# Kernel tuning notes

Measured on AMD Instinct MI355X. Metric: run time of the kernel, lower is better.

Reference implementation:

```python
import jax, jax.numpy as jnp
import numpy as np

F1, F2, F3 = 128, 64, 32
K = 16          # tensor_neurons
BINS = 16
FEAT = K + BINS # feature_count with histogram
BN1, BN2, BN3 = 16, 8, 4
NLAB = 128


def gcn(x, W, b, src, dst, n):
    # PyG GCNConv: h = x W; symmetric norm with self-loops; aggregate at dst.
    h = x @ W
    deg = jax.ops.segment_sum(jnp.ones(src.shape[0], h.dtype), dst, num_segments=n) + 1.0
    dinv = deg ** -0.5
    norm = (dinv[src] * dinv[dst])[:, None]
    agg = jax.ops.segment_sum(h[src] * norm, dst, num_segments=n)
    return agg + h * (dinv ** 2)[:, None] + b  # second term = self-loop


def conv_pass(feat, ei, w1, b1, w2, b2, w3, b3):
    n = feat.shape[0]
    src, dst = ei[0], ei[1]
    h = jax.nn.relu(gcn(feat, w1, b1, src, dst, n))
    h = jax.nn.relu(gcn(h, w2, b2, src, dst, n))
    return gcn(h, w3, b3, src, dst, n)  # [n, F3]


def att_pool(x, W):
    ctx = jnp.tanh(jnp.mean(x @ W, axis=0))      # [F3]
    sig = jax.nn.sigmoid(x @ ctx)                # [n]
    return x.T @ sig                             # [F3]


def histc_norm(a, b):
    # torch.histc with bins over [min, max] of the (detached) scores.
    s = jax.lax.stop_gradient(a @ b.T).reshape(-1)  # [N1*N2]
    lo, hi = s.min(), s.max()
    idx = jnp.clip(jnp.floor((s - lo) / jnp.maximum(hi - lo, 1e-12) * BINS).astype(jnp.int32), 0, BINS - 1)
    h = jax.ops.segment_sum(jnp.ones_like(s), idx, num_segments=BINS)
    return h / h.sum()


def setup_inputs() -> dict:
    key = jax.random.key(0)
    ks = jax.random.split(key, 24)
    N, E = 20000, 640000
    d = {
        'features_1': jax.random.normal(ks[0], (N, NLAB), jnp.float32),
        'features_2': jax.random.normal(ks[1], (N, NLAB), jnp.float32),
        'edge_index_1': jax.random.randint(ks[2], (2, E), 0, N),
        'edge_index_2': jax.random.randint(ks[3], (2, E), 0, N),
        'avg_v': jax.random.uniform(ks[4], (1,), jnp.float32) * 10.0 + 5.0,
    }
    def w(k, shape, fan_in):
        return jax.random.normal(k, shape, jnp.float32) * (1.0 / np.sqrt(fan_in))
    d['w1'] = w(ks[5], (NLAB, F1), NLAB); d['b1'] = jnp.zeros((F1,), jnp.float32)
    d['w2'] = w(ks[6], (F1, F2), F1);     d['b2'] = jnp.zeros((F2,), jnp.float32)
    d['w3'] = w(ks[7], (F2, F3), F2);     d['b3'] = jnp.zeros((F3,), jnp.float32)
    d['attn_w'] = w(ks[8], (F3, F3), F3)
    d['ntn_w'] = w(ks[9], (F3, F3, K), F3)
    d['ntn_v'] = w(ks[10], (K, 2 * F3), 2 * F3)
    d['ntn_b'] = jnp.zeros((K,), jnp.float32)
    d['fc1_w'] = w(ks[11], (FEAT, BN1), FEAT); d['fc1_b'] = jnp.zeros((BN1,), jnp.float32)
    d['fc2_w'] = w(ks[12], (BN1, BN2), BN1);   d['fc2_b'] = jnp.zeros((BN2,), jnp.float32)
    d['fc3_w'] = w(ks[13], (BN2, BN3), BN2);   d['fc3_b'] = jnp.zeros((BN3,), jnp.float32)
    d['score_w'] = w(ks[14], (BN3, 1), BN3);   d['score_b'] = jnp.zeros((1,), jnp.float32)
    return d


def reference(features_1, features_2, avg_v,
              w1, b1, w2, b2, w3, b3,
              attn_w, ntn_w, ntn_v, ntn_b,
              fc1_w, fc1_b, fc2_w, fc2_b, fc3_w, fc3_b,
              score_w, score_b,
              edge_index_1, edge_index_2):
    a1 = conv_pass(features_1, edge_index_1, w1, b1, w2, b2, w3, b3)  # [N1, F3]
    a2 = conv_pass(features_2, edge_index_2, w1, b1, w2, b2, w3, b3)  # [N2, F3]
    p1 = att_pool(a1, attn_w)  # [F3]
    p2 = att_pool(a2, attn_w)  # [F3]
    ntn = jax.nn.relu(jnp.einsum('i,ijk,j->k', p1, ntn_w, p2)
                      + ntn_v @ jnp.concatenate([p1, p2]) + ntn_b)  # [K]
    hist = histc_norm(a1, a2)  # [BINS]
    s = jnp.concatenate([ntn, hist])[None, :]  # [1, FEAT]
    s = jax.nn.relu(s @ fc1_w + fc1_b)
    s = jax.nn.relu(s @ fc2_w + fc2_b)
    s = jax.nn.relu(s @ fc3_w + fc3_b)
    score = jax.nn.sigmoid((s @ score_w + score_b).reshape(-1))  # [1]
    pre_ged = -jnp.log(score) * avg_v  # target_mode == 'exp'
    return score, pre_ged
```

## Files before the change

kernel.cpp:

```cpp
#include <hip/hip_runtime.h>


typedef short s16x8 __attribute__((ext_vector_type(8)));
typedef float f32x4 __attribute__((ext_vector_type(4)));


__global__ __launch_bounds__(256) void count_kern(const int* __restrict__ ei1,
                                                  const int* __restrict__ ei2,
                                                  int* counts, int N, int E)
{
    int g = blockIdx.y;
    const int* dst = (g ? ei2 : ei1) + E;
    int* cnt = counts + (size_t)g * N;
    for (int e = blockIdx.x * 256 + threadIdx.x; e < E; e += gridDim.x * 256)
        atomicAdd(&cnt[dst[e]], 1);
}

__global__ __launch_bounds__(256) void dinv_kern(const int* __restrict__ counts,
                                                 float* dinv, int N)
{
    int g = blockIdx.y;
    int i = blockIdx.x * 256 + threadIdx.x;
    if (i < N) dinv[(size_t)g * N + i] = 1.0f / sqrtf((float)counts[(size_t)g * N + i] + 1.0f);
}

__global__ __launch_bounds__(1024) void scan_kern(const int* __restrict__ counts,
                                                  int* row_ptr, int* cursor, int N)
{
    int g = blockIdx.x;
    const int* cnt = counts + (size_t)g * N;
    int* rp  = row_ptr + (size_t)g * (N + 1);
    int* cur = cursor  + (size_t)g * (N + 1);
    __shared__ int lds[1024];
    int t = threadIdx.x;
    int CH = (N + 1023) >> 10;
    int base = t * CH;
    int sum = 0;
    for (int i = 0; i < CH; i++) {
        int idx = base + i;
        if (idx < N) sum += cnt[idx];
    }
    lds[t] = sum;
    __syncthreads();
    for (int s = 1; s < 1024; s <<= 1) {
        int add = (t >= s) ? lds[t - s] : 0;
        __syncthreads();
        lds[t] += add;
        __syncthreads();
    }
    int run = lds[t] - sum;
    if (t == 0) rp[0] = 0;
    for (int i = 0; i < CH; i++) {
        int idx = base + i;
        if (idx < N) {
            int v = cnt[idx];
            cur[idx] = run;
            run += v;
            rp[idx + 1] = run;
        }
    }
}

__global__ __launch_bounds__(256) void scatter_kern(const int* __restrict__ ei1,
                                                    const int* __restrict__ ei2,
                                                    int* cursor, int* col, int N, int E)
{
    int g = blockIdx.y;
    const int* ei = g ? ei2 : ei1;
    const int* src = ei;
    const int* dst = ei + E;
    int* cur = cursor + (size_t)g * (N + 1);
    int* cl  = col    + (size_t)g * E;
    int e = blockIdx.x * 256 + threadIdx.x;
    if (e < E) {
        int pos = atomicAdd(&cur[dst[e]], 1);
        cl[pos] = src[e];
    }
}


template <int K, int NCOL>
__global__ __launch_bounds__(256) void gemm_kern(const float* __restrict__ xa,
                                                 const float* __restrict__ xb,
                                                 const float* __restrict__ W,
                                                 const float* __restrict__ dinva,
                                                 const float* __restrict__ dinvb,
                                                 float* ya, float* yb, int nodes)
{
    int g = blockIdx.y;
    const float* x = g ? xb : xa;
    const float* dinv = g ? dinvb : dinva;
    float* y = g ? yb : ya;
    constexpr int MB  = 32;
    constexpr int NG  = 256 / NCOL;
    constexpr int RPT = MB / NG;
    __shared__ float xs[MB][K];
    int row0 = blockIdx.x * MB;
    int t = threadIdx.x;
    constexpr int TOT = MB * K / 4;
    for (int i = t; i < TOT; i += 256) {
        int lin = i * 4;
        int r = lin / K, k = lin % K;
        float4 v = make_float4(0.f, 0.f, 0.f, 0.f);
        if (row0 + r < nodes) v = *(const float4*)&x[(size_t)(row0 + r) * K + k];
        *(float4*)&xs[r][k] = v;
    }
    __syncthreads();
    int c  = t % NCOL;
    int rg = t / NCOL;
    float acc[RPT];
#pragma unroll
    for (int i = 0; i < RPT; i++) acc[i] = 0.f;
    for (int k = 0; k < K; k++) {
        float w = W[k * NCOL + c];
#pragma unroll
        for (int i = 0; i < RPT; i++) acc[i] += xs[rg * RPT + i][k] * w;
    }
#pragma unroll
    for (int i = 0; i < RPT; i++) {
        int r = row0 + rg * RPT + i;
        if (r < nodes) y[(size_t)r * NCOL + c] = acc[i] * dinv[r];
    }
}


template <int F, bool RELU>
__global__ __launch_bounds__(256) void agg_kern(const float* __restrict__ ha,
                                                const float* __restrict__ hb,
                                                const int* __restrict__ colA,
                                                const int* __restrict__ colB,
                                                const int* __restrict__ rpA,
                                                const int* __restrict__ rpB,
                                                const float* __restrict__ dinvA,
                                                const float* __restrict__ dinvB,
                                                const float* __restrict__ bias,
                                                float* ya, float* yb, int nodes)
{
    int g = blockIdx.y;
    const float2* hp  = (const float2*)(g ? hb : ha);
    const int*   col  = g ? colB : colA;
    const int*   rp   = g ? rpB : rpA;
    const float* dinv = g ? dinvB : dinvA;
    float2* y = (float2*)(g ? yb : ya);
    constexpr int TPN = F / 2;
    constexpr int NPB = 256 / TPN;
    int t = threadIdx.x;
    int ni = blockIdx.x * NPB + t / TPN;
    int f2 = t % TPN;
    if (ni >= nodes) return;
    int e0 = rp[ni], e1 = rp[ni + 1];
    float ax = 0.f, ay = 0.f;
    for (int e = e0; e < e1; e++) {
        float2 v = hp[(size_t)col[e] * TPN + f2];
        ax += v.x; ay += v.y;
    }
    float2 self = hp[(size_t)ni * TPN + f2];
    float di = dinv[ni];
    float ox = di * (ax + self.x) + bias[2 * f2];
    float oy = di * (ay + self.y) + bias[2 * f2 + 1];
    if (RELU) { ox = fmaxf(ox, 0.f); oy = fmaxf(oy, 0.f); }
    y[(size_t)ni * TPN + f2] = make_float2(ox, oy);
}


__global__ __launch_bounds__(256) void colsum_kern(const float* __restrict__ a1,
                                                   const float* __restrict__ a2,
                                                   float* colsum, int nodes)
{
    int g = blockIdx.y;
    const float* a = g ? a2 : a1;
    float* cs = colsum + g * 32;
    int t = threadIdx.x;
    int c = t & 31, rr = t >> 5;
    float acc = 0.f;
    for (int r = blockIdx.x * 8 + rr; r < nodes; r += gridDim.x * 8)
        acc += a[(size_t)r * 32 + c];
    __shared__ float lds[256];
    lds[t] = acc;
    __syncthreads();
    if (t < 32) {
        float s = 0.f;
#pragma unroll
        for (int j = 0; j < 8; j++) s += lds[j * 32 + t];
        atomicAdd(&cs[t], s);
    }
}

__global__ void ctx_kern(const float* __restrict__ colsum, const float* __restrict__ W,
                         float* ctx, float invN)
{
    int g = blockIdx.x;
    const float* cs = colsum + g * 32;
    int c = threadIdx.x;
    float s = 0.f;
    for (int j = 0; j < 32; j++) s += cs[j] * invN * W[j * 32 + c];
    ctx[g * 32 + c] = tanhf(s);
}

__global__ __launch_bounds__(256) void pool_kern(const float* __restrict__ a1,
                                                 const float* __restrict__ a2,
                                                 const float* __restrict__ ctx,
                                                 float* pooled, int nodes)
{
    int g = blockIdx.y;
    const float* a  = g ? a2 : a1;
    const float* cx = ctx + g * 32;
    float* pl = pooled + g * 32;
    int t = threadIdx.x;
    int c = t & 31, rr = t >> 5;
    float cxc = cx[c];
    float acc = 0.f;
    for (int r = blockIdx.x * 8 + rr; r < nodes; r += gridDim.x * 8) {
        float v = a[(size_t)r * 32 + c];
        float d = v * cxc;
#pragma unroll
        for (int m = 16; m >= 1; m >>= 1) d += __shfl_xor(d, m, 32);
        acc += v * (1.f / (1.f + expf(-d)));
    }
    __shared__ float lds[256];
    lds[t] = acc;
    __syncthreads();
    if (t < 32) {
        float s = 0.f;
#pragma unroll
        for (int j = 0; j < 8; j++) s += lds[j * 32 + t];
        atomicAdd(&pl[t], s);
    }
}


__global__ __launch_bounds__(512) void ntn_kern(const float* __restrict__ pooled,
                                                const float* __restrict__ ntn_w,
                                                const float* __restrict__ ntn_v,
                                                const float* __restrict__ ntn_b,
                                                float* ntn)
{
    const float* p1 = pooled;
    const float* p2 = pooled + 32;
    __shared__ float lds[512];
    int t = threadIdx.x;
    int i = t >> 4, k = t & 15;
    float s = 0.f;
    for (int j = 0; j < 32; j++) s += ntn_w[(i * 32 + j) * 16 + k] * p2[j];
    lds[t] = s * p1[i];
    __syncthreads();
    if (t < 16) {
        float v = 0.f;
        for (int ii = 0; ii < 32; ii++) v += lds[ii * 16 + t];
        for (int j = 0; j < 32; j++) v += ntn_v[t * 64 + j] * p1[j];
        for (int j = 0; j < 32; j++) v += ntn_v[t * 64 + 32 + j] * p2[j];
        v += ntn_b[t];
        ntn[t] = fmaxf(v, 0.f);
    }
}


__device__ __forceinline__ unsigned encf(float f)
{
    unsigned b = __float_as_uint(f);
    return b ^ (unsigned)(((int)b >> 31) | 0x80000000);
}
__device__ __forceinline__ float decf(unsigned u)
{
    unsigned b = (u & 0x80000000u) ? (u ^ 0x80000000u) : ~u;
    return __uint_as_float(b);
}

__device__ __forceinline__ unsigned short f2bf(float f)
{
    unsigned u = __float_as_uint(f);
    return (unsigned short)((u + 0x7FFFu + ((u >> 16) & 1u)) >> 16);
}

__global__ __launch_bounds__(256) void split_kern(const float* __restrict__ a,
                                                  unsigned short* __restrict__ hi,
                                                  unsigned short* __restrict__ lo,
                                                  int total4)
{
    int i = blockIdx.x * 256 + threadIdx.x;
    if (i >= total4) return;
    float4 v = ((const float4*)a)[i];
    ushort4 h, l;
    h.x = f2bf(v.x); l.x = f2bf(v.x - __uint_as_float((unsigned)h.x << 16));
    h.y = f2bf(v.y); l.y = f2bf(v.y - __uint_as_float((unsigned)h.y << 16));
    h.z = f2bf(v.z); l.z = f2bf(v.z - __uint_as_float((unsigned)h.z << 16));
    h.w = f2bf(v.w); l.w = f2bf(v.w - __uint_as_float((unsigned)h.w << 16));
    ((ushort4*)hi)[i] = h;
    ((ushort4*)lo)[i] = l;
}

__device__ __forceinline__ s16x8 ldfrag(const unsigned short* __restrict__ base,
                                        int node0, int lane)
{
    const unsigned short* p = base + (size_t)(node0 + (lane & 15)) * 32 + 8 * (lane >> 4);
    return *(const s16x8*)p;
}

template <int PASS>
__global__ __launch_bounds__(256) void hist_pass(const unsigned short* __restrict__ h1,
                                                 const unsigned short* __restrict__ l1,
                                                 const unsigned short* __restrict__ h2,
                                                 const unsigned short* __restrict__ l2,
                                                 unsigned* encMinArr, unsigned* encMaxArr,
                                                 unsigned* histSub)
{
    int t = threadIdx.x, w = t >> 6, lane = t & 63;
    int row0 = blockIdx.x * 160 + (w >> 1) * 80;
    int col0 = blockIdx.y * 160 + (w & 1) * 80;
    __shared__ unsigned wh[(PASS == 1) ? 4 : 1][16][64];
    __shared__ float bc[2];
    __shared__ unsigned ru[4], rv[4];
    __shared__ float rf[4], rg[4];

    float scale = 0.f, nls = 0.f;
    if (PASS == 1) {
        for (int i = t; i < 4096; i += 256) ((unsigned*)wh)[i] = 0u;
        unsigned mnu = encMinArr[t];
        unsigned mxu = encMaxArr[t];
#pragma unroll
        for (int m = 32; m >= 1; m >>= 1) {
            unsigned a = (unsigned)__shfl_xor((int)mnu, m);
            unsigned b = (unsigned)__shfl_xor((int)mxu, m);
            mnu = a < mnu ? a : mnu;
            mxu = b > mxu ? b : mxu;
        }
        if (lane == 0) { ru[w] = mnu; rv[w] = mxu; }
        __syncthreads();
        if (t == 0) {
            mnu = ru[0]; mxu = rv[0];
#pragma unroll
            for (int j = 1; j < 4; j++) {
                mnu = ru[j] < mnu ? ru[j] : mnu;
                mxu = rv[j] > mxu ? rv[j] : mxu;
            }
            float lof = decf(mnu), hif = decf(mxu);
            bc[0] = lof;
            bc[1] = 16.f / fmaxf(hif - lof, 1e-12f);
        }
        __syncthreads();
        float lo = bc[0];
        scale = bc[1];
        nls = -lo * scale;
    }

    s16x8 ah[5], al[5];
#pragma unroll
    for (int r = 0; r < 5; r++) {
        ah[r] = ldfrag(h1, row0 + r * 16, lane);
        al[r] = ldfrag(l1, row0 + r * 16, lane);
    }
    float mn = 3.4e38f, mx = -3.4e38f;
#pragma unroll
    for (int c = 0; c < 5; c++) {
        s16x8 bh = ldfrag(h2, col0 + c * 16, lane);
        s16x8 bl = ldfrag(l2, col0 + c * 16, lane);
        f32x4 acc[5];
#pragma unroll
        for (int r = 0; r < 5; r++) {
            f32x4 z = {0.f, 0.f, 0.f, 0.f};
            z = __builtin_amdgcn_mfma_f32_16x16x32_bf16(ah[r], bh, z, 0, 0, 0);
            z = __builtin_amdgcn_mfma_f32_16x16x32_bf16(al[r], bh, z, 0, 0, 0);
            z = __builtin_amdgcn_mfma_f32_16x16x32_bf16(ah[r], bl, z, 0, 0, 0);
            acc[r] = z;
        }
#pragma unroll
        for (int r = 0; r < 5; r++)
#pragma unroll
            for (int j = 0; j < 4; j++) {
                float s = acc[r][j];
                if (PASS == 0) {
                    mn = fminf(mn, s);
                    mx = fmaxf(mx, s);
                } else {
                    int bi = (int)fminf(fmaxf(fmaf(s, scale, nls), 0.f), 15.f);
                    atomicAdd(&wh[w][bi][lane], 1u);
                }
            }
    }

    int slot = (int)((blockIdx.x * gridDim.y + blockIdx.y) & 255u);
    if (PASS == 0) {
#pragma unroll
        for (int m = 32; m >= 1; m >>= 1) {
            mn = fminf(mn, __shfl_xor(mn, m));
            mx = fmaxf(mx, __shfl_xor(mx, m));
        }
        if (lane == 0) { rf[w] = mn; rg[w] = mx; }
        __syncthreads();
        if (t == 0) {
            mn = fminf(fminf(rf[0], rf[1]), fminf(rf[2], rf[3]));
            mx = fmaxf(fmaxf(rg[0], rg[1]), fmaxf(rg[2], rg[3]));
            atomicMin(&encMinArr[slot], encf(mn));
            atomicMax(&encMaxArr[slot], encf(mx));
        }
    } else {
        __syncthreads();
        for (int s = 32; s > 0; s >>= 1) {
            for (int idx = t; idx < 4 * 16 * s; idx += 256) {
                int ww  = idx / (16 * s);
                int rem = idx - ww * 16 * s;
                int b   = rem / s;
                int l2i = rem - b * s;
                wh[ww][b][l2i] += wh[ww][b][l2i + s];
            }
            __syncthreads();
        }
        if (t < 16) {
            unsigned tot = wh[0][t][0] + wh[1][t][0] + wh[2][t][0] + wh[3][t][0];
            if (tot) atomicAdd(&histSub[slot * 16 + t], tot);
        }
    }
}


__global__ __launch_bounds__(256) void final_kern(const float* __restrict__ ntn,
                           const unsigned* __restrict__ histSub,
                           const float* __restrict__ fc1w, const float* __restrict__ fc1b,
                           const float* __restrict__ fc2w, const float* __restrict__ fc2b,
                           const float* __restrict__ fc3w, const float* __restrict__ fc3b,
                           const float* __restrict__ scw, const float* __restrict__ scb,
                           const float* __restrict__ avg_v, float* out)
{
    __shared__ unsigned part[256];
    __shared__ float s_fc1w[512];
    __shared__ float s_fc2w[128];
    __shared__ float s_fc3w[32];
    __shared__ float s_fc1b[16], s_fc2b[8], s_fc3b[4], s_scw[4];
    __shared__ float s_feat[32];
    __shared__ float s_h1[16], s_h2[8], s_h3[4];
    __shared__ float s_scb, s_avg, s_inv;
    int t = threadIdx.x;

    s_fc1w[t]       = fc1w[t];
    s_fc1w[t + 256] = fc1w[t + 256];
    if (t < 128)               s_fc2w[t] = fc2w[t];
    else if (t < 160)          s_fc3w[t - 128] = fc3w[t - 128];
    else if (t < 176)          s_fc1b[t - 160] = fc1b[t - 160];
    else if (t < 184)          s_fc2b[t - 176] = fc2b[t - 176];
    else if (t < 188)          s_fc3b[t - 184] = fc3b[t - 184];
    else if (t < 192)          s_scw[t - 188]  = scw[t - 188];
    else if (t < 208)          s_feat[t - 192] = ntn[t - 192];
    else if (t == 208)         s_scb = scb[0];
    else if (t == 209)         s_avg = avg_v[0];

    int b = t & 15, grp = t >> 4;
    unsigned s = 0;
    for (int i = grp; i < 256; i += 16) s += histSub[i * 16 + b];
    part[t] = s;
    __syncthreads();
    if (t < 16) {
        unsigned tot = 0;
#pragma unroll
        for (int j = 0; j < 16; j++) tot += part[j * 16 + t];
        part[t] = tot;
    }
    __syncthreads();
    if (t == 0) {
        float total = 0.f;
#pragma unroll
        for (int j = 0; j < 16; j++) total += (float)part[j];
        s_inv = 1.f / total;
    }
    __syncthreads();
    if (t < 16) s_feat[16 + t] = (float)part[t] * s_inv;
    __syncthreads();

    if (t < 16) {
        float s2 = s_fc1b[t];
#pragma unroll
        for (int i = 0; i < 32; i++) s2 += s_feat[i] * s_fc1w[i * 16 + t];
        s_h1[t] = fmaxf(s2, 0.f);
    }
    __syncthreads();
    if (t < 8) {
        float s2 = s_fc2b[t];
#pragma unroll
        for (int i = 0; i < 16; i++) s2 += s_h1[i] * s_fc2w[i * 8 + t];
        s_h2[t] = fmaxf(s2, 0.f);
    }
    __syncthreads();
    if (t < 4) {
        float s2 = s_fc3b[t];
#pragma unroll
        for (int i = 0; i < 8; i++) s2 += s_h2[i] * s_fc3w[i * 4 + t];
        s_h3[t] = fmaxf(s2, 0.f);
    }
    __syncthreads();
    if (t == 0) {
        float sc = s_scb;
#pragma unroll
        for (int i = 0; i < 4; i++) sc += s_h3[i] * s_scw[i];
        float score = 1.f / (1.f + expf(-sc));
        out[0] = score;
        out[1] = -logf(fmaxf(score, 1e-37f)) * s_avg;
    }
}


extern "C" void kernel_launch(void* const* d_in, const int* in_sizes, int n_in,
                              void* d_out, int out_size, void* d_ws, size_t ws_size,
                              hipStream_t stream)
{
    (void)n_in; (void)out_size; (void)ws_size;
    const float* feat1 = (const float*)d_in[0];
    const float* feat2 = (const float*)d_in[1];
    const int*   ei1   = (const int*)d_in[2];
    const int*   ei2   = (const int*)d_in[3];
    const float* avg_v = (const float*)d_in[4];
    const float* w1 = (const float*)d_in[5];
    const float* b1 = (const float*)d_in[6];
    const float* w2 = (const float*)d_in[7];
    const float* b2 = (const float*)d_in[8];
    const float* w3 = (const float*)d_in[9];
    const float* b3 = (const float*)d_in[10];
    const float* attn_w = (const float*)d_in[11];
    const float* ntn_w  = (const float*)d_in[12];
    const float* ntn_v  = (const float*)d_in[13];
    const float* ntn_b  = (const float*)d_in[14];
    const float* fc1w = (const float*)d_in[15];
    const float* fc1b = (const float*)d_in[16];
    const float* fc2w = (const float*)d_in[17];
    const float* fc2b = (const float*)d_in[18];
    const float* fc3w = (const float*)d_in[19];
    const float* fc3b = (const float*)d_in[20];
    const float* scw  = (const float*)d_in[21];
    const float* scb  = (const float*)d_in[22];

    const int N = in_sizes[0] / 128;
    const int E = in_sizes[2] / 2;

    char* ws = (char*)d_ws;
    size_t o = 0;
    auto take = [&](size_t bytes) -> void* {
        void* p = ws + o;
        o += (bytes + 255) & ~(size_t)255;
        return p;
    };
    size_t zbeg = o;
    int*      counts    = (int*)     take((size_t)2 * N * 4);
    float*    zero0     = (float*)   take(128 * 4);
    unsigned* histSub   = (unsigned*)take(256 * 16 * 4);
    unsigned* encMaxArr = (unsigned*)take(256 * 4);
    size_t zend = o;
    unsigned* encMinArr = (unsigned*)take(256 * 4);
    int*   rp   = (int*)  take((size_t)2 * (N + 1) * 4);
    int*   cur  = (int*)  take((size_t)2 * (N + 1) * 4);
    float* dinv = (float*)take((size_t)2 * N * 4);
    int*   col  = (int*)  take((size_t)2 * E * 4);
    float* bufA = (float*)take((size_t)2 * N * 128 * 4);
    float* bufB = (float*)take((size_t)2 * N * 128 * 4);
    float* aout = (float*)take((size_t)2 * N * 32 * 4);
    float* ctx  = (float*)take(64 * 4);
    float* ntn  = (float*)take(16 * 4);
    float* colsum = zero0;
    float* pooled = zero0 + 64;
    unsigned short* hiP = (unsigned short*)bufA;
    unsigned short* loP = hiP + (size_t)2 * N * 32;

    hipMemsetAsync(ws + zbeg, 0, zend - zbeg, stream);
    hipMemsetAsync(encMinArr, 0xFF, 256 * 4, stream);

    count_kern<<<dim3(512, 2), 256, 0, stream>>>(ei1, ei2, counts, N, E);
    dinv_kern<<<dim3((N + 255) / 256, 2), 256, 0, stream>>>(counts, dinv, N);
    scan_kern<<<2, 1024, 0, stream>>>(counts, rp, cur, N);
    scatter_kern<<<dim3((E + 255) / 256, 2), 256, 0, stream>>>(ei1, ei2, cur, col, N, E);

    float* bufA2 = bufA + (size_t)N * 128;
    float* bufB2 = bufB + (size_t)N * 128;
    float* a2p   = aout + (size_t)N * 32;
    const int* col2 = col + (size_t)E;
    const int* rp2  = rp + (N + 1);
    const float* dinv2 = dinv + N;

    gemm_kern<128, 128><<<dim3((N + 31) / 32, 2), 256, 0, stream>>>(feat1, feat2, w1, dinv, dinv2, bufB, bufB2, N);
    agg_kern<128, true><<<dim3((N + 3) / 4, 2), 256, 0, stream>>>(bufB, bufB2, col, col2, rp, rp2, dinv, dinv2, b1, bufA, bufA2, N);
    gemm_kern<128, 64><<<dim3((N + 31) / 32, 2), 256, 0, stream>>>(bufA, bufA2, w2, dinv, dinv2, bufB, bufB2, N);
    agg_kern<64, true><<<dim3((N + 7) / 8, 2), 256, 0, stream>>>(bufB, bufB2, col, col2, rp, rp2, dinv, dinv2, b2, bufA, bufA2, N);
    gemm_kern<64, 32><<<dim3((N + 31) / 32, 2), 256, 0, stream>>>(bufA, bufA2, w3, dinv, dinv2, bufB, bufB2, N);
    agg_kern<32, false><<<dim3((N + 15) / 16, 2), 256, 0, stream>>>(bufB, bufB2, col, col2, rp, rp2, dinv, dinv2, b3, aout, a2p, N);

    colsum_kern<<<dim3(64, 2), 256, 0, stream>>>(aout, a2p, colsum, N);
    ctx_kern<<<2, 32, 0, stream>>>(colsum, attn_w, ctx, 1.f / (float)N);
    pool_kern<<<dim3(64, 2), 256, 0, stream>>>(aout, a2p, ctx, pooled, N);

    ntn_kern<<<1, 512, 0, stream>>>(pooled, ntn_w, ntn_v, ntn_b, ntn);

    split_kern<<<(2 * N * 32 / 4 + 255) / 256, 256, 0, stream>>>(aout, hiP, loP, 2 * N * 32 / 4);
    unsigned short* hi2 = hiP + (size_t)N * 32;
    unsigned short* lo2 = loP + (size_t)N * 32;
    dim3 hgrid(N / 160, N / 160);
    hist_pass<0><<<hgrid, 256, 0, stream>>>(hiP, loP, hi2, lo2, encMinArr, encMaxArr, histSub);
    hist_pass<1><<<hgrid, 256, 0, stream>>>(hiP, loP, hi2, lo2, encMinArr, encMaxArr, histSub);

    final_kern<<<1, 256, 0, stream>>>(ntn, histSub, fc1w, fc1b, fc2w, fc2b, fc3w, fc3b,
                                      scw, scb, avg_v, (float*)d_out);
}
```

Measured before the change: 840.6 us.

## Fold histogram scale into pre-split operands and widen aggregation to float4

The aggregation kernel now loads float4 per thread and unrolls the neighbor loop by four, so each thread issues more independent gathers and handles fewer edges per feature. The histogram second pass no longer redoes the min/max reduction in every block. A small prep kernel computes the scale once, a second split pre-multiplies both operands by the scale, and the offset goes into the MFMA accumulator init, which removes the per-element fma. The cost is an extra split pass and a prep launch, and scaling before the bf16 split can change bin assignment slightly at bin edges.

```diff
diff --git a/kernel.cpp b/kernel.cpp
--- a/kernel.cpp
+++ b/kernel.cpp
@@ -137,29 +137,47 @@
                                                 float* ya, float* yb, int nodes)
 {
     int g = blockIdx.y;
-    const float2* hp  = (const float2*)(g ? hb : ha);
+    const float4* hp  = (const float4*)(g ? hb : ha);
     const int*   col  = g ? colB : colA;
     const int*   rp   = g ? rpB : rpA;
     const float* dinv = g ? dinvB : dinvA;
-    float2* y = (float2*)(g ? yb : ya);
-    constexpr int TPN = F / 2;
+    float4* y = (float4*)(g ? yb : ya);
+    constexpr int TPN = F / 4;
     constexpr int NPB = 256 / TPN;
     int t = threadIdx.x;
     int ni = blockIdx.x * NPB + t / TPN;
-    int f2 = t % TPN;
+    int f4 = t % TPN;
     if (ni >= nodes) return;
     int e0 = rp[ni], e1 = rp[ni + 1];
-    float ax = 0.f, ay = 0.f;
-    for (int e = e0; e < e1; e++) {
-        float2 v = hp[(size_t)col[e] * TPN + f2];
-        ax += v.x; ay += v.y;
-    }
-    float2 self = hp[(size_t)ni * TPN + f2];
+    float ax = 0.f, ay = 0.f, az = 0.f, aw = 0.f;
+    int e = e0;
+    for (; e + 4 <= e1; e += 4) {
+        int c0 = col[e], c1 = col[e + 1], c2 = col[e + 2], c3 = col[e + 3];
+        float4 v0 = hp[(size_t)c0 * TPN + f4];
+        float4 v1 = hp[(size_t)c1 * TPN + f4];
+        float4 v2 = hp[(size_t)c2 * TPN + f4];
+        float4 v3 = hp[(size_t)c3 * TPN + f4];
+        ax += (v0.x + v1.x) + (v2.x + v3.x);
+        ay += (v0.y + v1.y) + (v2.y + v3.y);
+        az += (v0.z + v1.z) + (v2.z + v3.z);
+        aw += (v0.w + v1.w) + (v2.w + v3.w);
+    }
+    for (; e < e1; e++) {
+        float4 v = hp[(size_t)col[e] * TPN + f4];
+        ax += v.x; ay += v.y; az += v.z; aw += v.w;
+    }
+    float4 self = hp[(size_t)ni * TPN + f4];
     float di = dinv[ni];
-    float ox = di * (ax + self.x) + bias[2 * f2];
-    float oy = di * (ay + self.y) + bias[2 * f2 + 1];
-    if (RELU) { ox = fmaxf(ox, 0.f); oy = fmaxf(oy, 0.f); }
-    y[(size_t)ni * TPN + f2] = make_float2(ox, oy);
+    float4 bv = ((const float4*)bias)[f4];
+    float ox = di * (ax + self.x) + bv.x;
+    float oy = di * (ay + self.y) + bv.y;
+    float oz = di * (az + self.z) + bv.z;
+    float ow = di * (aw + self.w) + bv.w;
+    if (RELU) {
+        ox = fmaxf(ox, 0.f); oy = fmaxf(oy, 0.f);
+        oz = fmaxf(oz, 0.f); ow = fmaxf(ow, 0.f);
+    }
+    y[(size_t)ni * TPN + f4] = make_float4(ox, oy, oz, ow);
 }
 
 
@@ -272,7 +290,9 @@
     return (unsigned short)((u + 0x7FFFu + ((u >> 16) & 1u)) >> 16);
 }
 
+template <int SCALED>
 __global__ __launch_bounds__(256) void split_kern(const float* __restrict__ a,
+                                                  const float* __restrict__ prep,
                                                   unsigned short* __restrict__ hi,
                                                   unsigned short* __restrict__ lo,
                                                   int total4)
@@ -280,6 +300,10 @@
     int i = blockIdx.x * 256 + threadIdx.x;
     if (i >= total4) return;
     float4 v = ((const float4*)a)[i];
+    if (SCALED) {
+        float sc = prep[1];
+        v.x *= sc; v.y *= sc; v.z *= sc; v.w *= sc;
+    }
     ushort4 h, l;
     h.x = f2bf(v.x); l.x = f2bf(v.x - __uint_as_float((unsigned)h.x << 16));
     h.y = f2bf(v.y); l.y = f2bf(v.y - __uint_as_float((unsigned)h.y << 16));
@@ -289,6 +313,38 @@
     ((ushort4*)lo)[i] = l;
 }
 
+__global__ void prep_kern(const unsigned* __restrict__ encMinArr,
+                          const unsigned* __restrict__ encMaxArr,
+                          float* __restrict__ prep)
+{
+    __shared__ unsigned ru[4], rv[4];
+    int t = threadIdx.x;
+    unsigned mnu = encMinArr[t];
+    unsigned mxu = encMaxArr[t];
+#pragma unroll
+    for (int m = 32; m >= 1; m >>= 1) {
+        unsigned a = (unsigned)__shfl_xor((int)mnu, m);
+        unsigned b = (unsigned)__shfl_xor((int)mxu, m);
+        mnu = a < mnu ? a : mnu;
+        mxu = b > mxu ? b : mxu;
+    }
+    if ((t & 63) == 0) { ru[t >> 6] = mnu; rv[t >> 6] = mxu; }
+    __syncthreads();
+    if (t == 0) {
+        mnu = ru[0]; mxu = rv[0];
+#pragma unroll
+        for (int j = 1; j < 4; j++) {
+            mnu = ru[j] < mnu ? ru[j] : mnu;
+            mxu = rv[j] > mxu ? rv[j] : mxu;
+        }
+        float lo = decf(mnu), hi = decf(mxu);
+        float scale = 16.f / fmaxf(hi - lo, 1e-12f);
+        prep[0] = lo;
+        prep[1] = scale;
+        prep[2] = -lo * scale;
+    }
+}
+
 __device__ __forceinline__ s16x8 ldfrag(const unsigned short* __restrict__ base,
                                         int node0, int lane)
 {
@@ -301,6 +357,7 @@
                                                  const unsigned short* __restrict__ l1,
                                                  const unsigned short* __restrict__ h2,
                                                  const unsigned short* __restrict__ l2,
+                                                 const float* __restrict__ prep,
                                                  unsigned* encMinArr, unsigned* encMaxArr,
                                                  unsigned* histSub)
 {
@@ -308,40 +365,15 @@
     int row0 = blockIdx.x * 160 + (w >> 1) * 80;
     int col0 = blockIdx.y * 160 + (w & 1) * 80;
     __shared__ unsigned wh[(PASS == 1) ? 4 : 1][16][64];
-    __shared__ float bc[2];
-    __shared__ unsigned ru[4], rv[4];
     __shared__ float rf[4], rg[4];
 
-    float scale = 0.f, nls = 0.f;
+    float nls = 0.f;
     if (PASS == 1) {
         for (int i = t; i < 4096; i += 256) ((unsigned*)wh)[i] = 0u;
-        unsigned mnu = encMinArr[t];
-        unsigned mxu = encMaxArr[t];
-#pragma unroll
-        for (int m = 32; m >= 1; m >>= 1) {
-            unsigned a = (unsigned)__shfl_xor((int)mnu, m);
-            unsigned b = (unsigned)__shfl_xor((int)mxu, m);
-            mnu = a < mnu ? a : mnu;
-            mxu = b > mxu ? b : mxu;
-        }
-        if (lane == 0) { ru[w] = mnu; rv[w] = mxu; }
+        nls = prep[2];
         __syncthreads();
-        if (t == 0) {
-            mnu = ru[0]; mxu = rv[0];
-#pragma unroll
-            for (int j = 1; j < 4; j++) {
-                mnu = ru[j] < mnu ? ru[j] : mnu;
-                mxu = rv[j] > mxu ? rv[j] : mxu;
-            }
-            float lof = decf(mnu), hif = decf(mxu);
-            bc[0] = lof;
-            bc[1] = 16.f / fmaxf(hif - lof, 1e-12f);
-        }
-        __syncthreads();
-        float lo = bc[0];
-        scale = bc[1];
-        nls = -lo * scale;
-    }
+    }
+    f32x4 cinit = {nls, nls, nls, nls};
 
     s16x8 ah[5], al[5];
 #pragma unroll
@@ -357,7 +389,7 @@
         f32x4 acc[5];
 #pragma unroll
         for (int r = 0; r < 5; r++) {
-            f32x4 z = {0.f, 0.f, 0.f, 0.f};
+            f32x4 z = cinit;
             z = __builtin_amdgcn_mfma_f32_16x16x32_bf16(ah[r], bh, z, 0, 0, 0);
             z = __builtin_amdgcn_mfma_f32_16x16x32_bf16(al[r], bh, z, 0, 0, 0);
             z = __builtin_amdgcn_mfma_f32_16x16x32_bf16(ah[r], bl, z, 0, 0, 0);
@@ -372,7 +404,7 @@
                     mn = fminf(mn, s);
                     mx = fmaxf(mx, s);
                 } else {
-                    int bi = (int)fminf(fmaxf(fmaf(s, scale, nls), 0.f), 15.f);
+                    int bi = (int)fminf(fmaxf(s, 0.f), 15.f);
                     atomicAdd(&wh[w][bi][lane], 1u);
                 }
             }
@@ -552,10 +584,13 @@
     float* aout = (float*)take((size_t)2 * N * 32 * 4);
     float* ctx  = (float*)take(64 * 4);
     float* ntn  = (float*)take(16 * 4);
+    float* prep = (float*)take(4 * 4);
     float* colsum = zero0;
     float* pooled = zero0 + 64;
-    unsigned short* hiP = (unsigned short*)bufA;
-    unsigned short* loP = hiP + (size_t)2 * N * 32;
+    unsigned short* hiP  = (unsigned short*)bufA;
+    unsigned short* loP  = hiP + (size_t)2 * N * 32;
+    unsigned short* hiS  = (unsigned short*)bufB;
+    unsigned short* loS  = hiS + (size_t)2 * N * 32;
 
     hipMemsetAsync(ws + zbeg, 0, zend - zbeg, stream);
     hipMemsetAsync(encMinArr, 0xFF, 256 * 4, stream);
@@ -573,11 +608,11 @@
     const float* dinv2 = dinv + N;
 
     gemm_kern<128, 128><<<dim3((N + 31) / 32, 2), 256, 0, stream>>>(feat1, feat2, w1, dinv, dinv2, bufB, bufB2, N);
-    agg_kern<128, true><<<dim3((N + 3) / 4, 2), 256, 0, stream>>>(bufB, bufB2, col, col2, rp, rp2, dinv, dinv2, b1, bufA, bufA2, N);
+    agg_kern<128, true><<<dim3((N + 7) / 8, 2), 256, 0, stream>>>(bufB, bufB2, col, col2, rp, rp2, dinv, dinv2, b1, bufA, bufA2, N);
     gemm_kern<128, 64><<<dim3((N + 31) / 32, 2), 256, 0, stream>>>(bufA, bufA2, w2, dinv, dinv2, bufB, bufB2, N);
-    agg_kern<64, true><<<dim3((N + 7) / 8, 2), 256, 0, stream>>>(bufB, bufB2, col, col2, rp, rp2, dinv, dinv2, b2, bufA, bufA2, N);
+    agg_kern<64, true><<<dim3((N + 15) / 16, 2), 256, 0, stream>>>(bufB, bufB2, col, col2, rp, rp2, dinv, dinv2, b2, bufA, bufA2, N);
     gemm_kern<64, 32><<<dim3((N + 31) / 32, 2), 256, 0, stream>>>(bufA, bufA2, w3, dinv, dinv2, bufB, bufB2, N);
-    agg_kern<32, false><<<dim3((N + 15) / 16, 2), 256, 0, stream>>>(bufB, bufB2, col, col2, rp, rp2, dinv, dinv2, b3, aout, a2p, N);
+    agg_kern<32, false><<<dim3((N + 31) / 32, 2), 256, 0, stream>>>(bufB, bufB2, col, col2, rp, rp2, dinv, dinv2, b3, aout, a2p, N);
 
     colsum_kern<<<dim3(64, 2), 256, 0, stream>>>(aout, a2p, colsum, N);
     ctx_kern<<<2, 32, 0, stream>>>(colsum, attn_w, ctx, 1.f / (float)N);
@@ -585,12 +620,17 @@
 
     ntn_kern<<<1, 512, 0, stream>>>(pooled, ntn_w, ntn_v, ntn_b, ntn);
 
-    split_kern<<<(2 * N * 32 / 4 + 255) / 256, 256, 0, stream>>>(aout, hiP, loP, 2 * N * 32 / 4);
-    unsigned short* hi2 = hiP + (size_t)N * 32;
-    unsigned short* lo2 = loP + (size_t)N * 32;
+    int tot4 = 2 * N * 32 / 4;
+    split_kern<0><<<(tot4 + 255) / 256, 256, 0, stream>>>(aout, prep, hiP, loP, tot4);
+    unsigned short* hiP2 = hiP + (size_t)N * 32;
+    unsigned short* loP2 = loP + (size_t)N * 32;
+    unsigned short* hiS2 = hiS + (size_t)N * 32;
+    unsigned short* loS2 = loS + (size_t)N * 32;
     dim3 hgrid(N / 160, N / 160);
-    hist_pass<0><<<hgrid, 256, 0, stream>>>(hiP, loP, hi2, lo2, encMinArr, encMaxArr, histSub);
-    hist_pass<1><<<hgrid, 256, 0, stream>>>(hiP, loP, hi2, lo2, encMinArr, encMaxArr, histSub);
+    hist_pass<0><<<hgrid, 256, 0, stream>>>(hiP, loP, hiP2, loP2, prep, encMinArr, encMaxArr, histSub);
+    prep_kern<<<1, 256, 0, stream>>>(encMinArr, encMaxArr, prep);
+    split_kern<1><<<(tot4 + 255) / 256, 256, 0, stream>>>(aout, prep, hiS, loS, tot4);
+    hist_pass<1><<<hgrid, 256, 0, stream>>>(hiS, loS, hiS2, loS2, prep, encMinArr, encMaxArr, histSub);
 
     final_kern<<<1, 256, 0, stream>>>(ntn, histSub, fc1w, fc1b, fc2w, fc2b, fc3w, fc3b,
                                       scw, scb, avg_v, (float*)d_out);
```

Result: faster. 728.3 us (-13.4%).
